# Optimization experiments

Hardware: AMD Instinct MI355X
Metric: run time of the kernel (lower is better)

## Reference

```python
import jax, jax.numpy as jnp
import numpy as np

B_, L_, DM, DI, DS, DTR, DC = 1, 2048, 2048, 4096, 16, 128, 4


def setup_inputs() -> dict:
    key = jax.random.key(0)
    ks = jax.random.split(key, 8)
    s = lambda k, shape, scale: jax.random.normal(k, shape, jnp.float32) * scale
    inp = {
        "hidden_states": s(ks[0], (B_, L_, DM), 1.0),
        "in_proj_weight": s(ks[1], (2 * DI, DM), DM ** -0.5),
        "conv1d_weight": s(ks[2], (DI, 1, DC), DC ** -0.5),
        "x_proj_weight": s(ks[3], (DTR + 2 * DS, DI), DI ** -0.5),
        "dt_proj_weight": s(ks[4], (DI, DTR), DTR ** -0.5),
        "out_proj_weight": s(ks[5], (DM, DI), DI ** -0.5),
    }
    # dt_proj_bias = inverse-softplus of dt ~ LogUniform[1e-3, 0.1] (as in init_dtprojbias)
    dt = jnp.exp(jax.random.uniform(ks[6], (DI,), jnp.float32) * (np.log(0.1) - np.log(0.001)) + np.log(0.001))
    dt = jnp.clip(dt, 1e-4, None)
    inp["dt_proj_bias"] = dt + jnp.log(-jnp.expm1(-dt))
    # A_log init: log of repeat(arange(1, d_state+1)) per d_inner row
    inp["A_log"] = jnp.log(jnp.tile(jnp.arange(1, DS + 1, dtype=jnp.float32), (DI, 1)))
    inp["D"] = jnp.ones((DI,), jnp.float32)
    return inp


def reference(hidden_states, in_proj_weight, conv1d_weight, x_proj_weight,
              dt_proj_weight, dt_proj_bias, A_log, D, out_proj_weight):
    b, l, dm = hidden_states.shape
    di, ds = A_log.shape
    # in_proj: [b,l,dm] -> xz [b, 2*di, l]
    xz = jnp.einsum('ed,bld->bel', in_proj_weight, hidden_states)
    x, z = xz[:, :di], xz[:, di:]
    # depthwise causal conv1d (pad left d_conv-1, no bias) + SiLU
    x = jax.lax.conv_general_dilated(
        x, conv1d_weight, window_strides=(1,), padding=[(DC - 1, 0)],
        dimension_numbers=('NCH', 'OIH', 'NCH'), feature_group_count=di)
    x = jax.nn.silu(x)  # [b, di, l]
    # x_proj -> dt, B, C
    x_dbl = jnp.einsum('pd,bdl->blp', x_proj_weight, x)  # [b,l,dtr+2*ds]
    dt, Bc, Cc = jnp.split(x_dbl, [DTR, DTR + ds], axis=-1)
    delta = jnp.einsum('dr,blr->bld', dt_proj_weight, dt) + dt_proj_bias
    delta = jax.nn.softplus(delta)  # delta_softplus=True, delta_bias applied
    A = -jnp.exp(A_log)  # [di, ds]
    u = jnp.transpose(x, (0, 2, 1))  # [b,l,di]

    def step(h, inputs):
        d_t, B_t, C_t, u_t = inputs  # [b,di],[b,ds],[b,ds],[b,di]
        dA = jnp.exp(d_t[..., None] * A)                      # [b,di,ds]
        h = h * dA + (d_t * u_t)[..., None] * B_t[:, None, :]  # [b,di,ds]
        y = jnp.einsum('bdn,bn->bd', h, C_t)
        return h, y

    h0 = jnp.zeros((b, di, ds), hidden_states.dtype)
    xs = (jnp.swapaxes(delta, 0, 1), jnp.swapaxes(Bc, 0, 1),
          jnp.swapaxes(Cc, 0, 1), jnp.swapaxes(u, 0, 1))
    _, ys = jax.lax.scan(step, h0, xs)          # [l,b,di]
    y = jnp.swapaxes(ys, 0, 1) + u * D          # skip term u*D
    y = y * jax.nn.silu(jnp.transpose(z, (0, 2, 1)))  # gate
    return jnp.einsum('md,bld->blm', out_proj_weight, y)
```

## Files before the change

### kernel.cpp

```cpp
#include <hip/hip_runtime.h>
#include <hip/hip_bf16.h>

#define LSEQ 2048
#define DMODEL 2048
#define DINNER 4096
#define DSTATE 16
#define DTRANK 128
#define DCONV 4
#define DXP (DTRANK + 2*DSTATE)
#define NCHUNK 64
#define LCHUNK (LSEQ / NCHUNK)
#define KSPLIT 16

using bf16 = __hip_bfloat16;
typedef __attribute__((ext_vector_type(8))) short short8;
typedef __attribute__((ext_vector_type(4))) float float4v;

__device__ __forceinline__ float b2f(bf16 v) { return __bfloat162float(v); }
__device__ __forceinline__ bf16 f2b(float v) { return __float2bfloat16(v); }
__device__ __forceinline__ float bl16(unsigned u) { return __uint_as_float(u << 16); }
__device__ __forceinline__ float bh16(unsigned u) { return __uint_as_float(u & 0xffff0000u); }

__device__ __forceinline__ short f2bs(float v) {
    bf16 b = __float2bfloat16(v);
    union { bf16 b; short s; } u; u.b = b; return u.s;
}

__device__ __forceinline__ float fsilu(float x) {
    return x * __builtin_amdgcn_rcpf(1.0f + __expf(-x));
}

__device__ __forceinline__ short8 ld8(const float* p) {
    float4v f0 = *(const float4v*)p;
    float4v f1 = *(const float4v*)(p + 4);
    short8 r;
    r[0] = f2bs(f0[0]); r[1] = f2bs(f0[1]); r[2] = f2bs(f0[2]); r[3] = f2bs(f0[3]);
    r[4] = f2bs(f1[0]); r[5] = f2bs(f1[1]); r[6] = f2bs(f1[2]); r[7] = f2bs(f1[3]);
    return r;
}
__device__ __forceinline__ short8 ld8(const bf16* p) { return *(const short8*)p; }

template<typename CT> __device__ __forceinline__ CT cvtC(float v);
template<> __device__ __forceinline__ bf16  cvtC<bf16>(float v)  { return f2b(v); }
template<> __device__ __forceinline__ float cvtC<float>(float v) { return v; }

template<typename T> __device__ __forceinline__ float cvtL(T v);
template<> __device__ __forceinline__ float cvtL<bf16>(bf16 v)   { return b2f(v); }
template<> __device__ __forceinline__ float cvtL<float>(float v) { return v; }

__device__ __forceinline__ void glds16(const bf16* g, void* lds_base) {
    __builtin_amdgcn_global_load_lds(
        (const __attribute__((address_space(1))) void*)g,
        (__attribute__((address_space(3))) void*)lds_base, 16, 0, 0);
}

__global__ __launch_bounds__(256) void cvt4(
    const float* __restrict__ s0, bf16* __restrict__ d0, int n0,
    const float* __restrict__ s1, bf16* __restrict__ d1, int n1,
    const float* __restrict__ s2, bf16* __restrict__ d2, int n2,
    const float* __restrict__ s3, bf16* __restrict__ d3, int n3)
{
    const int b = blockIdx.x;
    const int nb0 = n0 >> 11, nb1 = n1 >> 11, nb2 = n2 >> 11;
    const float* s; bf16* d; int i;
    if (b < nb0)                  { s = s0; d = d0; i = b * 2048; }
    else if (b < nb0 + nb1)       { s = s1; d = d1; i = (b - nb0) * 2048; }
    else if (b < nb0 + nb1 + nb2) { s = s2; d = d2; i = (b - nb0 - nb1) * 2048; }
    else                          { s = s3; d = d3; i = (b - nb0 - nb1 - nb2) * 2048; }
    i += threadIdx.x * 8;
    *(short8*)(d + i) = ld8(s + i);
}

__global__ __launch_bounds__(256) void cvt1(
    const float* __restrict__ src, bf16* __restrict__ dst, int n)
{
    int i = (blockIdx.x * 256 + threadIdx.x) * 8;
    if (i >= n) return;
    *(short8*)(dst + i) = ld8(src + i);
}

#define GBAR  __builtin_amdgcn_s_barrier()
#define VMW4  asm volatile("s_waitcnt vmcnt(4)" ::: "memory")
#define VMW0  asm volatile("s_waitcnt vmcnt(0)" ::: "memory")

#define LDA8(BASE, RB, AF) do {                                                \
  _Pragma("unroll") for (int mi_ = 0; mi_ < 4; ++mi_)                          \
  _Pragma("unroll") for (int kk_ = 0; kk_ < 2; ++kk_)                          \
    AF[mi_][kk_] = *(const short8*)((BASE) + (((RB) + mi_*16 + t16) << 6)      \
                                    + ((((kk_*4) + quad) ^ sw7) << 3));        \
} while (0)

#define LDB4(BASE, RB, BF) do {                                                \
  _Pragma("unroll") for (int nj_ = 0; nj_ < 2; ++nj_)                          \
  _Pragma("unroll") for (int kk_ = 0; kk_ < 2; ++kk_)                          \
    BF[nj_][kk_] = *(const short8*)((BASE) + (((RB) + nj_*16 + t16) << 6)      \
                                    + ((((kk_*4) + quad) ^ sw7) << 3));        \
} while (0)

#define MM16(AF, BF, MO, NO) do {                                              \
  _Pragma("unroll") for (int kk_ = 0; kk_ < 2; ++kk_)                          \
  _Pragma("unroll") for (int mi_ = 0; mi_ < 4; ++mi_)                          \
  _Pragma("unroll") for (int nj_ = 0; nj_ < 2; ++nj_)                          \
    acc[(MO)+mi_][(NO)+nj_] = __builtin_amdgcn_mfma_f32_16x16x32_bf16(         \
        AF[mi_][kk_], BF[nj_][kk_], acc[(MO)+mi_][(NO)+nj_], 0, 0, 0);         \
} while (0)

#define ST_ALO(tau) do { size_t ko_ = (size_t)(tau) << 6; int bo_ = ((tau)&1) << 15; \
  glds16(sA +       ko_, dA0 + bo_);                                           \
  glds16(sA + oA1 + ko_, dA1 + bo_); } while (0)
#define ST_AHI(tau) do { size_t ko_ = (size_t)(tau) << 6; int bo_ = ((tau)&1) << 15; \
  glds16(sA + oA2 + ko_, dA2 + bo_);                                           \
  glds16(sA + oA3 + ko_, dA3 + bo_); } while (0)
#define ST_BLO(tau) do { size_t ko_ = (size_t)(tau) << 6; int bo_ = ((tau)&1) << 15; \
  glds16(sB +       ko_, dB0 + bo_);                                           \
  glds16(sB + oB1 + ko_, dB1 + bo_); } while (0)
#define ST_BHI(tau) do { size_t ko_ = (size_t)(tau) << 6; int bo_ = ((tau)&1) << 15; \
  glds16(sB + oB2 + ko_, dB2 + bo_);                                           \
  glds16(sB + oB3 + ko_, dB3 + bo_); } while (0)

#define KSTEP(T, BI) do {                                                      \
    const bf16* Ab = As[BI];                                                   \
    const bf16* Bb = Bs[BI];                                                   \
    short8 af[4][2], b0[2][2], b1[2][2];                                       \
                                       \
    LDA8(Ab, wm, af);                                                          \
    LDB4(Bb, wn, b0);                                                          \
    if ((T) + 1 < NT) { ST_AHI((T) + 1); ST_BLO((T) + 1); }                    \
    __builtin_amdgcn_s_setprio(1); MM16(af, b0, 0, 0);                         \
    __builtin_amdgcn_s_setprio(0); GBAR;                                       \
                    \
    LDB4(Bb, wn + 32, b1);                                                     \
    if ((T) + 2 < NT) ST_ALO((T) + 2);                                         \
    __builtin_amdgcn_s_setprio(1); MM16(af, b1, 0, 2);                         \
    __builtin_amdgcn_s_setprio(0); GBAR;                                       \
                           \
    LDA8(Ab, wm + 64, af);                                                     \
    if ((T) + 2 < NT) ST_BHI((T) + 2);                                         \
    __builtin_amdgcn_s_setprio(1); MM16(af, b1, 4, 2);                         \
    __builtin_amdgcn_s_setprio(0); GBAR;                                       \
                                   \
    __builtin_amdgcn_s_setprio(1); MM16(af, b0, 4, 0);                         \
    __builtin_amdgcn_s_setprio(0);                                             \
    if ((T) + 2 < NT) { VMW4; } else { VMW0; }                                 \
    GBAR;                                                                      \
} while (0)

#define GEMM_PRO_COMMON                                                        \
    const int t    = threadIdx.x;                                              \
    const int wave = t >> 6;                                                   \
    const int lane = t & 63;                                                   \
    const int t16  = lane & 15;                                                \
    const int quad = lane >> 4;                                                \
    const int sw7  = t16 & 7;                                                  \
    const int wm   = (wave >> 2) * 128;                                        \
    const int wn   = (wave & 3) * 64;                                          \
    const int lrow  = lane >> 3;                                               \
    const int lseg  = lane & 7;                                                \
    const int segx  = (lseg ^ lrow) * 8;                                       \
    const int bwoff = (wave & 3) * 8 + (wave >> 2) * 64;

#define GEMM_LDS_DSTS                                                          \
    char* dA0 = (char*)&As[0][(  0 + wave * 8) * 64];                          \
    char* dA1 = (char*)&As[0][(128 + wave * 8) * 64];                          \
    char* dA2 = (char*)&As[0][( 64 + wave * 8) * 64];                          \
    char* dA3 = (char*)&As[0][(192 + wave * 8) * 64];                          \
    char* dB0 = (char*)&Bs[0][(  0 + bwoff) * 64];                             \
    char* dB1 = (char*)&Bs[0][(128 + bwoff) * 64];                             \
    char* dB2 = (char*)&Bs[0][( 32 + bwoff) * 64];                             \
    char* dB3 = (char*)&Bs[0][(160 + bwoff) * 64];

__global__ __launch_bounds__(512, 2) void gemm_inproj(
    const bf16* __restrict__ A, int lda,
    const bf16* __restrict__ B, int ldb,
    bf16* __restrict__ C, int ldc, int K)
{
    __shared__ __align__(16) bf16 As[2][256 * 64];
    __shared__ __align__(16) bf16 Bs[2][256 * 64];
    GEMM_PRO_COMMON
    const int bid = blockIdx.x;
    const int s   = (bid & 7) * (gridDim.x >> 3) + (bid >> 3);
    const int bm0 = (s & 7) << 8;
    const int bn0 = (s >> 3) << 8;

    const bf16* sA = A + (size_t)(bm0 + wave * 8 + lrow) * lda + segx;
    const bf16* sB = B + (size_t)(bn0 + bwoff + lrow) * ldb + segx;
    const size_t oA1 = (size_t)128 * lda, oA2 = (size_t)64 * lda, oA3 = (size_t)192 * lda;
    const size_t oB1 = (size_t)128 * ldb, oB2 = (size_t)32 * ldb, oB3 = (size_t)160 * ldb;
    GEMM_LDS_DSTS

    const int NT = K >> 6;

    float4v acc[8][4];
#pragma unroll
    for (int i = 0; i < 8; ++i)
#pragma unroll
        for (int j = 0; j < 4; ++j) acc[i][j] = (float4v)(0.0f);

    ST_ALO(0); ST_AHI(0); ST_BLO(0); ST_BHI(0);
    if (NT > 1) { ST_ALO(1); ST_BHI(1); VMW4; } else { VMW0; }
    GBAR;

    for (int T = 0; T < NT; T += 2) {
        KSTEP(T, 0);
        KSTEP(T + 1, 1);
    }

#pragma unroll
    for (int mi = 0; mi < 8; ++mi) {
#pragma unroll
        for (int nj = 0; nj < 4; ++nj) {
            const int m_base = bm0 + wm + (mi >> 2) * 64 + (mi & 3) * 16 + quad * 4;
            const int n_g    = bn0 + wn + (nj >> 1) * 32 + (nj & 1) * 16 + t16;
#pragma unroll
            for (int r = 0; r < 4; ++r)
                C[(size_t)(m_base + r) * ldc + n_g] = f2b(acc[mi][nj][r]);
        }
    }
}

__global__ __launch_bounds__(256) void gemm_outproj(
    const bf16* __restrict__ A, int lda,
    const bf16* __restrict__ B, int ldb,
    float* __restrict__ C, int ldc, int K)
{
    __shared__ bf16 As[128][64];
    __shared__ bf16 Bs[128][64];

    const int t    = threadIdx.x;
    const int wave = t >> 6;
    const int lane = t & 63;
    const int t16  = lane & 15;
    const int quad = lane >> 4;
    const int wm   = (wave >> 1) * 64;
    const int wn   = (wave & 1) * 64;

    const int bid = blockIdx.x;
    const int m_t = ((bid & 1) << 3) | ((bid >> 3) & 7);
    const int n_t = (((bid >> 1) & 3) << 2) | ((bid >> 6) & 3);
    const int bm0 = m_t << 7;
    const int bn0 = n_t << 7;

    const int lrow = lane >> 3;
    const int gseg = ((lane & 7) ^ lrow) * 8;

    const bf16* Ag[4]; char* Ad[4];
#pragma unroll
    for (int g = 0; g < 4; g++) {
        int r = wave * 32 + g * 8;
        Ag[g] = A + (size_t)(bm0 + r + lrow) * lda + gseg;
        Ad[g] = (char*)As + r * 128;
    }
    const bf16* Bg[4]; char* Bd[4];
#pragma unroll
    for (int g = 0; g < 4; g++) {
        int r = wave * 32 + g * 8;
        Bg[g] = B + (size_t)(bn0 + r + lrow) * ldb + gseg;
        Bd[g] = (char*)Bs + r * 128;
    }

    float4v acc[4][4];
#pragma unroll
    for (int i = 0; i < 4; i++)
#pragma unroll
        for (int j = 0; j < 4; j++) acc[i][j] = (float4v)(0.0f);

    const int sw = t16 & 7;

    for (int k0 = 0; k0 < K; k0 += 64) {
        __syncthreads();
#pragma unroll
        for (int g = 0; g < 4; g++) glds16(Ag[g] + k0, Ad[g]);
#pragma unroll
        for (int g = 0; g < 4; g++) glds16(Bg[g] + k0, Bd[g]);
        __syncthreads();

#pragma unroll
        for (int kk = 0; kk < 2; kk++) {
            const int kso = ((kk * 4 + quad) ^ sw) * 8;
            short8 a[4], b[4];
#pragma unroll
            for (int mi = 0; mi < 4; mi++)
                a[mi] = *(const short8*)(&As[wm + mi * 16 + t16][kso]);
#pragma unroll
            for (int nj = 0; nj < 4; nj++)
                b[nj] = *(const short8*)(&Bs[wn + nj * 16 + t16][kso]);
#pragma unroll
            for (int mi = 0; mi < 4; mi++)
#pragma unroll
                for (int nj = 0; nj < 4; nj++)
                    acc[mi][nj] = __builtin_amdgcn_mfma_f32_16x16x32_bf16(
                        a[mi], b[nj], acc[mi][nj], 0, 0, 0);
        }
    }

#pragma unroll
    for (int mi = 0; mi < 4; mi++) {
#pragma unroll
        for (int nj = 0; nj < 4; nj++) {
            int n_g = bn0 + wn + nj * 16 + t16;
#pragma unroll
            for (int r = 0; r < 4; r++) {
                int m_g = bm0 + wm + mi * 16 + quad * 4 + r;
                C[(size_t)m_g * ldc + n_g] = acc[mi][nj][r];
            }
        }
    }
}

__global__ __launch_bounds__(256) void gemm_xproj(
    const bf16* __restrict__ A, int lda,
    const bf16* __restrict__ B, int ldb,
    float* __restrict__ P)
{
    __shared__ bf16 As[128][64];
    __shared__ bf16 Bs[160][64];

    const int t    = threadIdx.x;
    const int wave = t >> 6;
    const int lane = t & 63;
    const int t16  = lane & 15;
    const int quad = lane >> 4;
    const int wm   = (wave >> 1) * 64;
    const int wn   = (wave & 1) * 80;
    const int bm0  = blockIdx.x * 128;
    const int kbeg = blockIdx.y * (DINNER / KSPLIT);

    const int lrow = lane >> 3;
    const int gseg = ((lane & 7) ^ lrow) * 8;

    const bf16* Ag[4]; char* Ad[4];
#pragma unroll
    for (int g = 0; g < 4; g++) {
        int r = wave * 32 + g * 8;
        Ag[g] = A + (size_t)(bm0 + r + lrow) * lda + gseg + kbeg;
        Ad[g] = (char*)As + r * 128;
    }
    const bf16* Bg[5]; char* Bd[5];
#pragma unroll
    for (int g = 0; g < 5; g++) {
        int r = wave * 40 + g * 8;
        Bg[g] = B + (size_t)(r + lrow) * ldb + gseg + kbeg;
        Bd[g] = (char*)Bs + r * 128;
    }

    float4v acc[4][5];
#pragma unroll
    for (int i = 0; i < 4; i++)
#pragma unroll
        for (int j = 0; j < 5; j++) acc[i][j] = (float4v)(0.0f);

    const int sw = t16 & 7;

    for (int k0 = 0; k0 < DINNER / KSPLIT; k0 += 64) {
        __syncthreads();
#pragma unroll
        for (int g = 0; g < 4; g++) glds16(Ag[g] + k0, Ad[g]);
#pragma unroll
        for (int g = 0; g < 5; g++) glds16(Bg[g] + k0, Bd[g]);
        __syncthreads();

#pragma unroll
        for (int kk = 0; kk < 2; kk++) {
            const int kso = ((kk * 4 + quad) ^ sw) * 8;
            short8 a[4], b[5];
#pragma unroll
            for (int mi = 0; mi < 4; mi++)
                a[mi] = *(const short8*)(&As[wm + mi * 16 + t16][kso]);
#pragma unroll
            for (int nj = 0; nj < 5; nj++)
                b[nj] = *(const short8*)(&Bs[wn + nj * 16 + t16][kso]);
#pragma unroll
            for (int mi = 0; mi < 4; mi++)
#pragma unroll
                for (int nj = 0; nj < 5; nj++)
                    acc[mi][nj] = __builtin_amdgcn_mfma_f32_16x16x32_bf16(
                        a[mi], b[nj], acc[mi][nj], 0, 0, 0);
        }
    }

    float* Pk = P + (size_t)blockIdx.y * LSEQ * DXP;
#pragma unroll
    for (int mi = 0; mi < 4; mi++) {
#pragma unroll
        for (int nj = 0; nj < 5; nj++) {
            int n_g = wn + nj * 16 + t16;
#pragma unroll
            for (int r = 0; r < 4; r++) {
                int m_g = bm0 + wm + mi * 16 + quad * 4 + r;
                Pk[(size_t)m_g * DXP + n_g] = acc[mi][nj][r];
            }
        }
    }
}

template<int BN, typename CT, bool SP>
__global__ __launch_bounds__(256) void gemm_glds64(
    const bf16* __restrict__ A, int lda,
    const bf16* __restrict__ B, int ldb,
    CT* __restrict__ C, int ldc,
    int K, const float* __restrict__ bias)
{
    constexpr int NJ  = BN / 32;
    constexpr int BGL = BN / 32;
    __shared__ bf16 As[128][64];
    __shared__ bf16 Bs[BN][64];

    const int t    = threadIdx.x;
    const int wave = t >> 6;
    const int lane = t & 63;
    const int t16  = lane & 15;
    const int quad = lane >> 4;
    const int wm   = (wave >> 1) * 64;
    const int wn   = (wave & 1) * (BN / 2);
    const int bm0  = blockIdx.x * 128;
    const int bn0  = blockIdx.y * BN;

    const int lrow = lane >> 3;
    const int gseg = (((lane & 7) ^ lrow) * 8);

    const bf16* Ag[4]; char* Ad[4];
#pragma unroll
    for (int g = 0; g < 4; g++) {
        Ag[g] = A + (size_t)(bm0 + wave * 32 + g * 8 + lrow) * lda + gseg;
        Ad[g] = (char*)As + (wave * 32 + g * 8) * 128;
    }
    const bf16* Bg[BGL]; char* Bd[BGL];
#pragma unroll
    for (int g = 0; g < BGL; g++) {
        int r = (BN == 128) ? (wave * 32 + g * 8) : (wave * 16 + g * 8);
        Bg[g] = B + (size_t)(bn0 + r + lrow) * ldb + gseg;
        Bd[g] = (char*)Bs + r * 128;
    }

    float4v acc[4][NJ];
#pragma unroll
    for (int i = 0; i < 4; i++)
#pragma unroll
        for (int j = 0; j < NJ; j++) acc[i][j] = (float4v)(0.0f);

    const int sw = t16 & 7;

    for (int k0 = 0; k0 < K; k0 += 64) {
        __syncthreads();
#pragma unroll
        for (int g = 0; g < 4; g++)   glds16(Ag[g] + k0, Ad[g]);
#pragma unroll
        for (int g = 0; g < BGL; g++) glds16(Bg[g] + k0, Bd[g]);
        __syncthreads();

#pragma unroll
        for (int kk = 0; kk < 2; kk++) {
            const int kso = ((kk * 4 + quad) ^ sw) * 8;
            short8 a[4], b[NJ];
#pragma unroll
            for (int mi = 0; mi < 4; mi++)
                a[mi] = *(const short8*)(&As[wm + mi * 16 + t16][kso]);
#pragma unroll
            for (int nj = 0; nj < NJ; nj++)
                b[nj] = *(const short8*)(&Bs[wn + nj * 16 + t16][kso]);
#pragma unroll
            for (int mi = 0; mi < 4; mi++)
#pragma unroll
                for (int nj = 0; nj < NJ; nj++)
                    acc[mi][nj] = __builtin_amdgcn_mfma_f32_16x16x32_bf16(
                        a[mi], b[nj], acc[mi][nj], 0, 0, 0);
        }
    }

#pragma unroll
    for (int mi = 0; mi < 4; mi++) {
#pragma unroll
        for (int nj = 0; nj < NJ; nj++) {
            int n_g = bn0 + wn + nj * 16 + t16;
            float bia = SP ? bias[n_g] : 0.0f;
#pragma unroll
            for (int r = 0; r < 4; r++) {
                int m_g = bm0 + wm + mi * 16 + quad * 4 + r;
                float v = acc[mi][nj][r];
                if (SP) {
                    float x = v + bia;
                    v = (x > 20.0f) ? x : __logf(1.0f + __expf(x));
                }
                C[(size_t)m_g * ldc + n_g] = cvtC<CT>(v);
            }
        }
    }
}

template<typename AT, typename CT, bool SP>
__global__ __launch_bounds__(256) void gemm_bt(
    const AT* __restrict__ A, int lda,
    const float* __restrict__ B, int ldb,
    CT* __restrict__ C, int ldc,
    int M, int N, int K,
    const float* __restrict__ bias)
{
    __shared__ bf16 As[64][40];
    __shared__ bf16 Bs[64][40];

    const int t    = threadIdx.x;
    const int bm0  = blockIdx.x * 64;
    const int bn0  = blockIdx.y * 64;
    const int row  = t >> 2;
    const int seg  = (t & 3) * 8;
    const int wave = t >> 6;
    const int lane = t & 63;
    const int wm   = (wave >> 1) * 32;
    const int wn   = (wave & 1) * 32;
    const int t16  = lane & 15;
    const int quad = lane >> 4;

    float4v acc[2][2];
#pragma unroll
    for (int i = 0; i < 2; i++)
#pragma unroll
        for (int j = 0; j < 2; j++) acc[i][j] = (float4v)(0.0f);

    const AT*    Aptr = A + (size_t)(bm0 + row) * lda + seg;
    const float* Bptr = B + (size_t)(bn0 + row) * ldb + seg;
    const bool a_ok = (bm0 + row) < M;
    const bool b_ok = (bn0 + row) < N;
    const short8 zero8 = (short8)(0);

    for (int k0 = 0; k0 < K; k0 += 32) {
        short8 av = a_ok ? ld8(Aptr + k0) : zero8;
        short8 bv = b_ok ? ld8(Bptr + k0) : zero8;
        __syncthreads();
        *(short8*)(&As[row][seg]) = av;
        *(short8*)(&Bs[row][seg]) = bv;
        __syncthreads();

        short8 a0 = *(const short8*)(&As[wm + t16][quad * 8]);
        short8 a1 = *(const short8*)(&As[wm + 16 + t16][quad * 8]);
        short8 b0 = *(const short8*)(&Bs[wn + t16][quad * 8]);
        short8 b1 = *(const short8*)(&Bs[wn + 16 + t16][quad * 8]);
        acc[0][0] = __builtin_amdgcn_mfma_f32_16x16x32_bf16(a0, b0, acc[0][0], 0, 0, 0);
        acc[0][1] = __builtin_amdgcn_mfma_f32_16x16x32_bf16(a0, b1, acc[0][1], 0, 0, 0);
        acc[1][0] = __builtin_amdgcn_mfma_f32_16x16x32_bf16(a1, b0, acc[1][0], 0, 0, 0);
        acc[1][1] = __builtin_amdgcn_mfma_f32_16x16x32_bf16(a1, b1, acc[1][1], 0, 0, 0);
    }

#pragma unroll
    for (int i = 0; i < 2; i++) {
#pragma unroll
        for (int j = 0; j < 2; j++) {
            int n_g = bn0 + wn + j * 16 + t16;
            if (n_g >= N) continue;
            float bia = SP ? bias[n_g] : 0.0f;
#pragma unroll
            for (int r = 0; r < 4; r++) {
                int m_g = bm0 + wm + i * 16 + quad * 4 + r;
                if (m_g >= M) continue;
                float v = acc[i][j][r];
                if (SP) {
                    float x = v + bia;
                    v = (x > 20.0f) ? x : log1pf(__expf(x));
                }
                C[(size_t)m_g * ldc + n_g] = cvtC<CT>(v);
            }
        }
    }
}

__global__ __launch_bounds__(256) void reduce_splitk(
    const float* __restrict__ P, bf16* __restrict__ C, float* __restrict__ bc, int MN)
{
    int i = blockIdx.x * 256 + threadIdx.x;
    if (i >= MN) return;
    float s = 0.f;
#pragma unroll
    for (int ks = 0; ks < KSPLIT; ks++) s += P[(size_t)ks * MN + i];
    C[i] = f2b(s);
    int l = i / DXP;
    int p = i - l * DXP;
    if (p >= DTRANK) bc[l * 32 + (p - DTRANK)] = s;
}

__global__ __launch_bounds__(256) void conv_silu_par(
    const bf16* __restrict__ xz, const float* __restrict__ w, bf16* __restrict__ xc)
{
    const int d  = blockIdx.x * 256 + threadIdx.x;
    const int lc = blockIdx.y * 64;
    const float w0 = w[d * 4 + 0];
    const float w1 = w[d * 4 + 1];
    const float w2 = w[d * 4 + 2];
    const float w3 = w[d * 4 + 3];
    const size_t S = 2 * DINNER;
    const bf16* p = xz + d;
    float xm3 = 0.f, xm2 = 0.f, xm1 = 0.f;
    if (lc >= 3) {
        xm3 = b2f(p[(size_t)(lc - 3) * S]);
        xm2 = b2f(p[(size_t)(lc - 2) * S]);
        xm1 = b2f(p[(size_t)(lc - 1) * S]);
    }
    for (int l = lc; l < lc + 64; ++l) {
        float x0 = b2f(p[(size_t)l * S]);
        float a = w0 * xm3 + w1 * xm2 + w2 * xm1 + w3 * x0;
        xc[(size_t)l * DINNER + d] = f2b(fsilu(a));
        xm3 = xm2; xm2 = xm1; xm1 = x0;
    }
}

__global__ __launch_bounds__(256) void conv_silu_inplace(
    bf16* __restrict__ xz, const float* __restrict__ w)
{
    const int d = blockIdx.x * 256 + threadIdx.x;
    const float w0 = w[d * 4 + 0];
    const float w1 = w[d * 4 + 1];
    const float w2 = w[d * 4 + 2];
    const float w3 = w[d * 4 + 3];
    bf16* p = xz + d;
    const size_t S = 2 * DINNER;
    float xm3 = 0.f, xm2 = 0.f, xm1 = 0.f;
    for (int l = 0; l < LSEQ; l += 4) {
        float x0 = b2f(p[(size_t)(l + 0) * S]);
        float x1 = b2f(p[(size_t)(l + 1) * S]);
        float x2 = b2f(p[(size_t)(l + 2) * S]);
        float x3 = b2f(p[(size_t)(l + 3) * S]);
        float a0 = w0 * xm3 + w1 * xm2 + w2 * xm1 + w3 * x0;
        float a1 = w0 * xm2 + w1 * xm1 + w2 * x0  + w3 * x1;
        float a2 = w0 * xm1 + w1 * x0  + w2 * x1  + w3 * x2;
        float a3 = w0 * x0  + w1 * x1  + w2 * x2  + w3 * x3;
        p[(size_t)(l + 0) * S] = f2b(a0 / (1.0f + __expf(-a0)));
        p[(size_t)(l + 1) * S] = f2b(a1 / (1.0f + __expf(-a1)));
        p[(size_t)(l + 2) * S] = f2b(a2 / (1.0f + __expf(-a2)));
        p[(size_t)(l + 3) * S] = f2b(a3 / (1.0f + __expf(-a3)));
        xm3 = x1; xm2 = x2; xm1 = x3;
    }
}

__global__ __launch_bounds__(256) void scan_chunk1(
    const float* __restrict__ dlt, const bf16* __restrict__ xc,
    const float* __restrict__ bc, const float* __restrict__ A_log,
    float* __restrict__ hend, float* __restrict__ Pbuf)
{
    const int d = blockIdx.x * 256 + threadIdx.x;
    const int c = blockIdx.y;

    float Ac[16];
    {
        const float* ap = A_log + d * DSTATE;
#pragma unroll
        for (int i = 0; i < 16; i++) Ac[i] = -__expf(ap[i]);
    }

    float h[16];
#pragma unroll
    for (int i = 0; i < 16; i++) h[i] = 0.f;
    float sdelta = 0.f;

    const float* pd = dlt + (size_t)c * LCHUNK * DINNER + d;
    const bf16*  pu = xc  + (size_t)c * LCHUNK * DINNER + d;
    const float* pb = bc  + (size_t)c * LCHUNK * 32;

#pragma unroll 2
    for (int l = 0; l < LCHUNK; ++l) {
        const float delta = *pd;
        const float u     = b2f(*pu);
        const float du    = delta * u;
        sdelta += delta;
        float4v B0 = *(const float4v*)pb;
        float4v B1 = *(const float4v*)(pb + 4);
        float4v B2 = *(const float4v*)(pb + 8);
        float4v B3 = *(const float4v*)(pb + 12);
#pragma unroll
        for (int i = 0; i < 16; i++) {
            float dA = __expf(delta * Ac[i]);
            float Bi = (i < 4) ? B0[i] : (i < 8) ? B1[i - 4] : (i < 12) ? B2[i - 8] : B3[i - 12];
            h[i] = h[i] * dA + du * Bi;
        }
        pd += DINNER; pu += DINNER; pb += 32;
    }

    float* hp = hend + ((size_t)c * DINNER + d) * DSTATE;
    float* pp = Pbuf + ((size_t)c * DINNER + d) * DSTATE;
#pragma unroll
    for (int q = 0; q < 4; q++) {
        float4v hv, pv;
#pragma unroll
        for (int j = 0; j < 4; j++) {
            hv[j] = h[q * 4 + j];
            pv[j] = __expf(sdelta * Ac[q * 4 + j]);
        }
        *(float4v*)(hp + q * 4) = hv;
        *(float4v*)(pp + q * 4) = pv;
    }
}

__global__ __launch_bounds__(256) void scan_combine(
    float* __restrict__ hend, const float* __restrict__ Pbuf)
{
    const int dn = blockIdx.x * 256 + threadIdx.x;
    const size_t STR = (size_t)DINNER * DSTATE;
    float H = 0.f;
    size_t idx = dn;
    for (int c0 = 0; c0 < NCHUNK; c0 += 8) {
        float he[8], pp[8];
#pragma unroll
        for (int j = 0; j < 8; j++) {
            he[j] = hend[idx + (size_t)j * STR];
            pp[j] = Pbuf[idx + (size_t)j * STR];
        }
#pragma unroll
        for (int j = 0; j < 8; j++) {
            hend[idx + (size_t)j * STR] = H;
            H = he[j] + pp[j] * H;
        }
        idx += 8 * STR;
    }
}

__global__ __launch_bounds__(256) void scan_chunk2(
    const float* __restrict__ dlt, const bf16* __restrict__ xc,
    bf16* __restrict__ xz, const float* __restrict__ bc,
    const float* __restrict__ A_log, const float* __restrict__ Dp,
    const float* __restrict__ Hin)
{
    const int d = blockIdx.x * 256 + threadIdx.x;
    const int c = blockIdx.y;

    float Ac[16];
    {
        const float* ap = A_log + d * DSTATE;
#pragma unroll
        for (int i = 0; i < 16; i++) Ac[i] = -__expf(ap[i]);
    }
    const float Dv = Dp[d];

    float h[16];
    {
        const float* hp = Hin + ((size_t)c * DINNER + d) * DSTATE;
#pragma unroll
        for (int q = 0; q < 4; q++) {
            float4v hv = *(const float4v*)(hp + q * 4);
#pragma unroll
            for (int j = 0; j < 4; j++) h[q * 4 + j] = hv[j];
        }
    }

    const float* pd = dlt + (size_t)c * LCHUNK * DINNER + d;
    const bf16*  pu = xc  + (size_t)c * LCHUNK * DINNER + d;
    const float* pb = bc  + (size_t)c * LCHUNK * 32;
    bf16*        pz = xz  + (size_t)c * LCHUNK * (2 * DINNER) + DINNER + d;

#pragma unroll 2
    for (int l = 0; l < LCHUNK; ++l) {
        const float delta = *pd;
        const float u     = b2f(*pu);
        const float du    = delta * u;
        float4v B0 = *(const float4v*)pb;
        float4v B1 = *(const float4v*)(pb + 4);
        float4v B2 = *(const float4v*)(pb + 8);
        float4v B3 = *(const float4v*)(pb + 12);
        float4v C0 = *(const float4v*)(pb + 16);
        float4v C1 = *(const float4v*)(pb + 20);
        float4v C2 = *(const float4v*)(pb + 24);
        float4v C3 = *(const float4v*)(pb + 28);
        float yv = 0.f;
#pragma unroll
        for (int i = 0; i < 16; i++) {
            float dA = __expf(delta * Ac[i]);
            float Bi = (i < 4) ? B0[i] : (i < 8) ? B1[i - 4] : (i < 12) ? B2[i - 8] : B3[i - 12];
            float Ci = (i < 4) ? C0[i] : (i < 8) ? C1[i - 4] : (i < 12) ? C2[i - 8] : C3[i - 12];
            h[i] = h[i] * dA + du * Bi;
            yv += h[i] * Ci;
        }
        yv += u * Dv;
        float z = b2f(*pz);
        yv *= fsilu(z);
        *pz = f2b(yv);
        pd += DINNER; pu += DINNER; pb += 32; pz += 2 * DINNER;
    }
}

template<typename DT>
__global__ __launch_bounds__(256) void scan_serial(
    const DT* __restrict__ dlt, bf16* __restrict__ xz,
    const bf16* __restrict__ xdbl,
    const float* __restrict__ A_log, const float* __restrict__ Dp)
{
    const int nq = threadIdx.x & 3;
    const int d  = blockIdx.x * 64 + (threadIdx.x >> 2);
    float Ac[4];
#pragma unroll
    for (int i = 0; i < 4; i++)
        Ac[i] = -__expf(A_log[d * DSTATE + nq * 4 + i]);
    const float Dv = Dp[d];
    float h[4] = {0.f, 0.f, 0.f, 0.f};
    for (int l = 0; l < LSEQ; ++l) {
        const float delta = cvtL<DT>(dlt[(size_t)l * DINNER + d]);
        const float u     = b2f(xz[(size_t)l * (2 * DINNER) + d]);
        const uint2 qb = *(const uint2*)(xdbl + (size_t)l * DXP + DTRANK + nq * 4);
        const uint2 qc = *(const uint2*)(xdbl + (size_t)l * DXP + DTRANK + DSTATE + nq * 4);
        float Bv[4] = { bl16(qb.x), bh16(qb.x), bl16(qb.y), bh16(qb.y) };
        float Cv[4] = { bl16(qc.x), bh16(qc.x), bl16(qc.y), bh16(qc.y) };
        const float du = delta * u;
        float yv = 0.f;
#pragma unroll
        for (int i = 0; i < 4; i++) {
            float dA = __expf(delta * Ac[i]);
            h[i] = h[i] * dA + du * Bv[i];
            yv += h[i] * Cv[i];
        }
        yv += __shfl_xor(yv, 1);
        yv += __shfl_xor(yv, 2);
        if (nq == 0) {
            yv += u * Dv;
            bf16* zp = xz + (size_t)l * (2 * DINNER) + DINNER + d;
            float z = b2f(*zp);
            yv *= z / (1.0f + __expf(-z));
            *zp = f2b(yv);
        }
    }
}

extern "C" void kernel_launch(void* const* d_in, const int* in_sizes, int n_in,
                              void* d_out, int out_size, void* d_ws, size_t ws_size,
                              hipStream_t stream)
{
    const float* hs      = (const float*)d_in[0];
    const float* w_in    = (const float*)d_in[1];
    const float* w_conv  = (const float*)d_in[2];
    const float* w_xproj = (const float*)d_in[3];
    const float* w_dt    = (const float*)d_in[4];
    const float *w_out, *b_dt, *A_log, *Dp;
    if (in_sizes[5] == DMODEL * DINNER) {
        w_out = (const float*)d_in[5];
        b_dt  = (const float*)d_in[6];
        A_log = (const float*)d_in[7];
        Dp    = (const float*)d_in[8];
    } else {
        b_dt  = (const float*)d_in[5];
        A_log = (const float*)d_in[6];
        Dp    = (const float*)d_in[7];
        w_out = (const float*)d_in[8];
    }
    float* out = (float*)d_out;

    const size_t SZ_XZ   = (size_t)LSEQ * 2 * DINNER * sizeof(bf16);
    const size_t SZ_XC   = (size_t)LSEQ * DINNER * sizeof(bf16);
    const size_t SZ_XDBL = (size_t)LSEQ * DXP * sizeof(bf16);
    const size_t SZ_DLTF = (size_t)LSEQ * DINNER * sizeof(float);
    const size_t SZ_HP   = (size_t)NCHUNK * DINNER * DSTATE * sizeof(float);
    const size_t SZ_BC   = (size_t)LSEQ * 32 * sizeof(float);

    char* p = (char*)d_ws;
    bf16* xz = (bf16*)p; p += SZ_XZ;

    const size_t need_fast = SZ_XZ + SZ_XC + SZ_XDBL + SZ_DLTF + 2 * SZ_HP + SZ_BC;
    const bool fast = ws_size >= need_fast;

    dim3 blk(256);

    if (fast) {
        bf16*  xc   = (bf16*)p;  p += SZ_XC;
        bf16*  xdbl = (bf16*)p;  p += SZ_XDBL;
        char*  hpr  = p;         p += SZ_DLTF;
        char*  dreg = p;
        float* dlt  = (float*)hpr;
        float* hend = (float*)dreg;
        float* Pbuf = (float*)(dreg + SZ_HP);
        float* bcb  = (float*)(dreg + 2 * SZ_HP);

        bf16*  w_in_b  = (bf16*)hpr;
        float* xp_part = (float*)hpr;
        bf16*  hs_b    = (bf16*)dreg;
        bf16*  w_dt_b  = (bf16*)(dreg + (size_t)LSEQ * DMODEL * sizeof(bf16));
        bf16*  w_xp_b  = (bf16*)(dreg + (size_t)LSEQ * DMODEL * sizeof(bf16)
                                      + (size_t)DINNER * DTRANK * sizeof(bf16));
        bf16*  w_out_b = (bf16*)xc;

        {
            int n0 = 2 * DINNER * DMODEL, n1 = LSEQ * DMODEL;
            int n2 = DINNER * DTRANK,     n3 = DXP * DINNER;
            cvt4<<<dim3((n0 + n1 + n2 + n3) / 2048), blk, 0, stream>>>(
                w_in, w_in_b, n0, hs, hs_b, n1, w_dt, w_dt_b, n2, w_xproj, w_xp_b, n3);
        }

        gemm_inproj<<<dim3(256), dim3(512), 0, stream>>>(
            hs_b, DMODEL, w_in_b, DMODEL, xz, 2*DINNER, DMODEL);

        conv_silu_par<<<dim3(DINNER/256, LSEQ/64), blk, 0, stream>>>(xz, w_conv, xc);

        gemm_xproj<<<dim3(LSEQ/128, KSPLIT), blk, 0, stream>>>(
            xc, DINNER, w_xp_b, DINNER, xp_part);
        reduce_splitk<<<dim3((LSEQ * DXP + 255) / 256), blk, 0, stream>>>(
            xp_part, xdbl, bcb, LSEQ * DXP);

        gemm_glds64<128, float, true><<<dim3(LSEQ/128, DINNER/128), blk, 0, stream>>>(
            xdbl, DXP, w_dt_b, DTRANK, dlt, DINNER, DTRANK, b_dt);

        scan_chunk1<<<dim3(DINNER/256, NCHUNK), blk, 0, stream>>>(
            dlt, xc, bcb, A_log, hend, Pbuf);
        scan_combine<<<dim3(DINNER*DSTATE/256), blk, 0, stream>>>(hend, Pbuf);
        scan_chunk2<<<dim3(DINNER/256, NCHUNK), blk, 0, stream>>>(
            dlt, xc, xz, bcb, A_log, Dp, hend);

        cvt1<<<dim3((DMODEL*DINNER)/2048), blk, 0, stream>>>(w_out, w_out_b, DMODEL*DINNER);
        gemm_outproj<<<dim3(256), blk, 0, stream>>>(
            xz + DINNER, 2*DINNER, w_out_b, DINNER, out, DMODEL, DINNER);
    } else {
        bf16* xdbl = (bf16*)p; p += SZ_XDBL;
        size_t used = (size_t)(p - (char*)d_ws);
        bool dlt_f32 = (ws_size - used) >= SZ_DLTF;

        gemm_bt<float, bf16, false><<<dim3(LSEQ/64, (2*DINNER)/64), blk, 0, stream>>>(
            hs, DMODEL, w_in, DMODEL, xz, 2*DINNER, LSEQ, 2*DINNER, DMODEL, nullptr);
        conv_silu_inplace<<<dim3(DINNER/256), blk, 0, stream>>>(xz, w_conv);
        gemm_bt<bf16, bf16, false><<<dim3(LSEQ/64, 3), blk, 0, stream>>>(
            xz, 2*DINNER, w_xproj, DINNER, xdbl, DXP, LSEQ, DXP, DINNER, nullptr);
        if (dlt_f32) {
            float* dlt = (float*)p;
            gemm_bt<bf16, float, true><<<dim3(LSEQ/64, DINNER/64), blk, 0, stream>>>(
                xdbl, DXP, w_dt, DTRANK, dlt, DINNER, LSEQ, DINNER, DTRANK, b_dt);
            scan_serial<float><<<dim3(DINNER/64), blk, 0, stream>>>(dlt, xz, xdbl, A_log, Dp);
        } else {
            bf16* dlt = (bf16*)p;
            gemm_bt<bf16, bf16, true><<<dim3(LSEQ/64, DINNER/64), blk, 0, stream>>>(
                xdbl, DXP, w_dt, DTRANK, dlt, DINNER, LSEQ, DINNER, DTRANK, b_dt);
            scan_serial<bf16><<<dim3(DINNER/64), blk, 0, stream>>>(dlt, xz, xdbl, A_log, Dp);
        }
        gemm_bt<bf16, float, false><<<dim3(LSEQ/64, DMODEL/64), blk, 0, stream>>>(
            xz + DINNER, 2*DINNER, w_out, DINNER, out, DMODEL, LSEQ, DMODEL, DINNER, nullptr);
    }
}
```

Measured before the change: 413.0 us.

## Triple-buffer out_proj GEMM with async prefetch and use exp2 in scan

Rewrites the out_proj GEMM main loop to use three LDS buffers, issuing global-to-LDS loads two K-tiles ahead with partial vmcnt waits and a single barrier per step. MFMA sections run at raised wave priority. This is meant to hide global load latency behind matrix math. Separately, the chunked scan kernels fold log2(e) into A once so each decay uses exp2f instead of __expf, saving a multiply per element. The triple buffer uses 96KB LDS and launch_bounds(256,1), which may lower occupancy.

```diff
diff --git a/kernel.cpp b/kernel.cpp
--- a/kernel.cpp
+++ b/kernel.cpp
@@ -81,6 +81,7 @@
 
 #define GBAR  __builtin_amdgcn_s_barrier()
 #define VMW4  asm volatile("s_waitcnt vmcnt(4)" ::: "memory")
+#define VMW8  asm volatile("s_waitcnt vmcnt(8)" ::: "memory")
 #define VMW0  asm volatile("s_waitcnt vmcnt(0)" ::: "memory")
 
 #define LDA8(BASE, RB, AF) do {                                                \
@@ -218,19 +219,50 @@
     }
 }
 
-__global__ __launch_bounds__(256) void gemm_outproj(
+#define OST(tau, BI) do { size_t ko_ = (size_t)(tau) << 6;                     \
+  _Pragma("unroll") for (int g_ = 0; g_ < 4; ++g_) {                           \
+    glds16(Ag[g_] + ko_, Ad[g_] + (BI) * 16384);                               \
+    glds16(Bg[g_] + ko_, Bd[g_] + (BI) * 16384); } } while (0)
+
+#define OKSTEP(T, BI) do {                                                     \
+    const bf16* Ab = &As[BI][0];                                               \
+    const bf16* Bb = &Bs[BI][0];                                               \
+    short8 a_[4][2], b_[4][2];                                                 \
+    _Pragma("unroll") for (int mi_ = 0; mi_ < 4; ++mi_)                        \
+    _Pragma("unroll") for (int kk_ = 0; kk_ < 2; ++kk_)                        \
+      a_[mi_][kk_] = *(const short8*)(Ab + ((wm + mi_*16 + t16) << 6)          \
+                                      + ((((kk_*4) + quad) ^ sw) << 3));       \
+    _Pragma("unroll") for (int nj_ = 0; nj_ < 4; ++nj_)                        \
+    _Pragma("unroll") for (int kk_ = 0; kk_ < 2; ++kk_)                        \
+      b_[nj_][kk_] = *(const short8*)(Bb + ((wn + nj_*16 + t16) << 6)          \
+                                      + ((((kk_*4) + quad) ^ sw) << 3));       \
+    if ((T) + 2 < NT) OST((T) + 2, ((BI) + 2) % 3);                            \
+    __builtin_amdgcn_s_setprio(1);                                             \
+    _Pragma("unroll") for (int kk_ = 0; kk_ < 2; ++kk_)                        \
+    _Pragma("unroll") for (int mi_ = 0; mi_ < 4; ++mi_)                        \
+    _Pragma("unroll") for (int nj_ = 0; nj_ < 4; ++nj_)                        \
+      acc[mi_][nj_] = __builtin_amdgcn_mfma_f32_16x16x32_bf16(                 \
+          a_[mi_][kk_], b_[nj_][kk_], acc[mi_][nj_], 0, 0, 0);                 \
+    __builtin_amdgcn_s_setprio(0);                                             \
+    if ((T) + 2 < NT) { VMW8; }                                                \
+    else if ((T) + 1 < NT) { VMW0; }                                           \
+    GBAR;                                                                      \
+} while (0)
+
+__global__ __launch_bounds__(256, 1) void gemm_outproj(
     const bf16* __restrict__ A, int lda,
     const bf16* __restrict__ B, int ldb,
     float* __restrict__ C, int ldc, int K)
 {
-    __shared__ bf16 As[128][64];
-    __shared__ bf16 Bs[128][64];
+    __shared__ __align__(16) bf16 As[3][128 * 64];
+    __shared__ __align__(16) bf16 Bs[3][128 * 64];
 
     const int t    = threadIdx.x;
     const int wave = t >> 6;
     const int lane = t & 63;
     const int t16  = lane & 15;
     const int quad = lane >> 4;
+    const int sw   = t16 & 7;
     const int wm   = (wave >> 1) * 64;
     const int wn   = (wave & 1) * 64;
 
@@ -248,15 +280,17 @@
     for (int g = 0; g < 4; g++) {
         int r = wave * 32 + g * 8;
         Ag[g] = A + (size_t)(bm0 + r + lrow) * lda + gseg;
-        Ad[g] = (char*)As + r * 128;
+        Ad[g] = (char*)&As[0][0] + r * 128;
     }
     const bf16* Bg[4]; char* Bd[4];
 #pragma unroll
     for (int g = 0; g < 4; g++) {
         int r = wave * 32 + g * 8;
         Bg[g] = B + (size_t)(bn0 + r + lrow) * ldb + gseg;
-        Bd[g] = (char*)Bs + r * 128;
-    }
+        Bd[g] = (char*)&Bs[0][0] + r * 128;
+    }
+
+    const int NT = K >> 6;
 
     float4v acc[4][4];
 #pragma unroll
@@ -264,34 +298,17 @@
 #pragma unroll
         for (int j = 0; j < 4; j++) acc[i][j] = (float4v)(0.0f);
 
-    const int sw = t16 & 7;
-
-    for (int k0 = 0; k0 < K; k0 += 64) {
-        __syncthreads();
-#pragma unroll
-        for (int g = 0; g < 4; g++) glds16(Ag[g] + k0, Ad[g]);
-#pragma unroll
-        for (int g = 0; g < 4; g++) glds16(Bg[g] + k0, Bd[g]);
-        __syncthreads();
-
-#pragma unroll
-        for (int kk = 0; kk < 2; kk++) {
-            const int kso = ((kk * 4 + quad) ^ sw) * 8;
-            short8 a[4], b[4];
-#pragma unroll
-            for (int mi = 0; mi < 4; mi++)
-                a[mi] = *(const short8*)(&As[wm + mi * 16 + t16][kso]);
-#pragma unroll
-            for (int nj = 0; nj < 4; nj++)
-                b[nj] = *(const short8*)(&Bs[wn + nj * 16 + t16][kso]);
-#pragma unroll
-            for (int mi = 0; mi < 4; mi++)
-#pragma unroll
-                for (int nj = 0; nj < 4; nj++)
-                    acc[mi][nj] = __builtin_amdgcn_mfma_f32_16x16x32_bf16(
-                        a[mi], b[nj], acc[mi][nj], 0, 0, 0);
-        }
-    }
+    OST(0, 0);
+    OST(1, 1);
+    VMW8;
+    GBAR;
+
+    for (int T = 0; T + 2 < NT; T += 3) {
+        OKSTEP(T, 0);
+        OKSTEP(T + 1, 1);
+        OKSTEP(T + 2, 2);
+    }
+    OKSTEP(NT - 1, 0);
 
 #pragma unroll
     for (int mi = 0; mi < 4; mi++) {
@@ -629,6 +646,8 @@
     }
 }
 
+#define LOG2E 1.44269504088896340736f
+
 __global__ __launch_bounds__(256) void scan_chunk1(
     const float* __restrict__ dlt, const bf16* __restrict__ xc,
     const float* __restrict__ bc, const float* __restrict__ A_log,
@@ -641,7 +660,7 @@
     {
         const float* ap = A_log + d * DSTATE;
 #pragma unroll
-        for (int i = 0; i < 16; i++) Ac[i] = -__expf(ap[i]);
+        for (int i = 0; i < 16; i++) Ac[i] = -__expf(ap[i]) * LOG2E;
     }
 
     float h[16];
@@ -665,7 +684,7 @@
         float4v B3 = *(const float4v*)(pb + 12);
 #pragma unroll
         for (int i = 0; i < 16; i++) {
-            float dA = __expf(delta * Ac[i]);
+            float dA = exp2f(delta * Ac[i]);
             float Bi = (i < 4) ? B0[i] : (i < 8) ? B1[i - 4] : (i < 12) ? B2[i - 8] : B3[i - 12];
             h[i] = h[i] * dA + du * Bi;
         }
@@ -680,7 +699,7 @@
 #pragma unroll
         for (int j = 0; j < 4; j++) {
             hv[j] = h[q * 4 + j];
-            pv[j] = __expf(sdelta * Ac[q * 4 + j]);
+            pv[j] = exp2f(sdelta * Ac[q * 4 + j]);
         }
         *(float4v*)(hp + q * 4) = hv;
         *(float4v*)(pp + q * 4) = pv;
@@ -723,7 +742,7 @@
     {
         const float* ap = A_log + d * DSTATE;
 #pragma unroll
-        for (int i = 0; i < 16; i++) Ac[i] = -__expf(ap[i]);
+        for (int i = 0; i < 16; i++) Ac[i] = -__expf(ap[i]) * LOG2E;
     }
     const float Dv = Dp[d];
 
@@ -759,7 +778,7 @@
         float yv = 0.f;
 #pragma unroll
         for (int i = 0; i < 16; i++) {
-            float dA = __expf(delta * Ac[i]);
+            float dA = exp2f(delta * Ac[i]);
             float Bi = (i < 4) ? B0[i] : (i < 8) ? B1[i - 4] : (i < 12) ? B2[i - 8] : B3[i - 12];
             float Ci = (i < 4) ? C0[i] : (i < 8) ? C1[i - 4] : (i < 12) ? C2[i - 8] : C3[i - 12];
             h[i] = h[i] * dA + du * Bi;
```

Result: no change. 418.6 us (+1.4%).
